# Kernel tuning notes

Measured on AMD Instinct MI355X. Metric: run time of the kernel, lower is better.

Reference implementation:

```python
import jax, jax.numpy as jnp
import numpy as np

N, E = 50000, 400000
IN_DIM, EDGE_F, OUT_DIM, EDGE_OUT, H = 256, 64, 32, 64, 8
ALPHA, TEMP, EPS = 0.2, 1.0, 1e-5


def lrelu(x):
    return jax.nn.leaky_relu(x, negative_slope=ALPHA)


def batch_norm(x, gamma, beta):
    # torch BatchNorm1d training-mode: biased variance over the batch dim
    mu = x.mean(0)
    var = x.var(0)
    return (x - mu) * jax.lax.rsqrt(var + EPS) * gamma + beta


def setup_inputs() -> dict:
    key = jax.random.key(0)
    ks = jax.random.split(key, 16)
    s = 0.05
    return {
        "node_inputs": jax.random.normal(ks[0], (N, IN_DIM), jnp.float32),
        "edge_inputs": jax.random.normal(ks[1], (E, EDGE_F), jnp.float32),
        "fc_w": jax.random.normal(ks[2], (IN_DIM, H * OUT_DIM), jnp.float32) * s,
        "attn_l": jax.random.normal(ks[3], (H, OUT_DIM), jnp.float32) * s,
        "attn_r": jax.random.normal(ks[4], (H, OUT_DIM), jnp.float32) * s,
        "ae_w1": jax.random.normal(ks[5], (EDGE_F, OUT_DIM), jnp.float32) * s,
        "ae_b1": jnp.zeros((OUT_DIM,), jnp.float32),
        "ae_w2": jax.random.normal(ks[6], (OUT_DIM, H), jnp.float32) * s,
        "ae_b2": jnp.zeros((H,), jnp.float32),
        "bn_n_g": jnp.ones((H * OUT_DIM,), jnp.float32),
        "bn_n_b": jnp.zeros((H * OUT_DIM,), jnp.float32),
        "eu_node_w": jax.random.normal(ks[7], (2 * H * OUT_DIM, EDGE_OUT), jnp.float32) * s,
        "eu_edge_w": jax.random.normal(ks[8], (EDGE_F, EDGE_OUT), jnp.float32) * s,
        "eu_final_w": jax.random.normal(ks[9], (2 * EDGE_OUT, EDGE_OUT), jnp.float32) * s,
        "bn_e_g": jnp.ones((EDGE_OUT,), jnp.float32),
        "bn_e_b": jnp.zeros((EDGE_OUT,), jnp.float32),
        "src": jax.random.randint(ks[10], (E,), 0, N, jnp.int32),
        "dst": jax.random.randint(ks[11], (E,), 0, N, jnp.int32),
    }


def reference(node_inputs, edge_inputs, fc_w, attn_l, attn_r, ae_w1, ae_b1, ae_w2,
              ae_b2, bn_n_g, bn_n_b, eu_node_w, eu_edge_w, eu_final_w, bn_e_g,
              bn_e_b, src, dst):
    # node projection, per-head attention scalars (dropout prob = 0 -> identity)
    ft = (node_inputs @ fc_w).reshape(N, H, OUT_DIM)          # [N,H,D]
    a1 = jnp.einsum('nhd,hd->nh', ft, attn_l)                 # [N,H]
    a2 = jnp.einsum('nhd,hd->nh', ft, attn_r)                 # [N,H]
    # edge-feature attention MLP: Linear -> LeakyReLU -> Linear
    e_attn = lrelu(edge_inputs @ ae_w1 + ae_b1) @ ae_w2 + ae_b2  # [E,H]
    a = lrelu(a1[src] + a2[dst] + e_attn) * TEMP              # [E,H]
    # two-pass edge softmax over incoming edges (segment by dst)
    a_max = jax.ops.segment_max(a, dst, num_segments=N)       # [N,H]
    a = jnp.exp(a - a_max[dst])                               # [E,H]
    z = jax.ops.segment_sum(a, dst, num_segments=N)           # [N,H]
    # weighted message aggregation
    msg = ft[src] * a[:, :, None]                             # [E,H,D]
    agg = jax.ops.segment_sum(msg, dst, num_segments=N)       # [N,H,D]
    z_safe = jnp.where(z == 0, 1.0, z)
    node_out = (agg / z_safe[:, :, None]).reshape(N, H * OUT_DIM)
    node_out = node_out + node_inputs                         # residual (dims match)
    node_out = batch_norm(lrelu(node_out), bn_n_g, bn_n_b)
    # edge update MLP
    node_f = lrelu(jnp.concatenate([node_out[src], node_out[dst]], -1) @ eu_node_w)
    edge_f = lrelu(edge_inputs @ eu_edge_w)
    edge_out = jnp.concatenate([node_f, edge_f], -1) @ eu_final_w
    edge_out = edge_out + edge_inputs                         # residual (dims match)
    edge_out = batch_norm(lrelu(edge_out), bn_e_g, bn_e_b)
    return node_out, edge_out
```

## Files before the change

### kernel.cpp

```cpp
#include <hip/hip_runtime.h>
#include <hip/hip_bf16.h>

typedef __hip_bfloat16 bf16;

#define N_NODES 50000
#define N_EDGES 400000
#define IN_DIM  256
#define EDGE_F  64
#define OUT_DIM 32
#define EDGE_OUT 64
#define NHEADS  8
#define HD      256
#define ALPHA   0.2f
#define BN_EPS  1e-5f

#define NBINS 50432
#define NBLK  197

__device__ __forceinline__ float b2f(bf16 v){ return __bfloat162float(v); }
__device__ __forceinline__ bf16  f2b(float v){ return __float2bfloat16(v); }
__device__ __forceinline__ float lrelu(float x){ return x > 0.f ? x : ALPHA*x; }
__device__ __forceinline__ unsigned fenc(float f){ unsigned u=__float_as_uint(f); return (u&0x80000000u)? ~u : (u|0x80000000u); }
__device__ __forceinline__ float fdec(unsigned k){ return (k&0x80000000u)? __uint_as_float(k&0x7fffffffu) : __uint_as_float(~k); }

template<bool F32> __device__ __forceinline__ float LD(const void* p, long i){
  if constexpr (F32) return ((const float*)p)[i];
  else               return b2f(((const bf16*)p)[i]);
}
template<bool F32> __device__ __forceinline__ void ST(void* p, long i, float v){
  if constexpr (F32) ((float*)p)[i] = v;
  else               ((bf16*)p)[i] = f2b(v);
}
template<bool F32> __device__ __forceinline__ void* ESEC(void* out){
  return (char*)out + (size_t)N_NODES*HD*(F32?4:2);
}

typedef __attribute__((ext_vector_type(8))) short bf16x8;
typedef __attribute__((ext_vector_type(4))) float f32x4;

union PackU { uint4 u; bf16x8 v; };
__device__ __forceinline__ bf16x8 as_frag(uint4 w){ PackU p; p.u = w; return p.v; }
__device__ __forceinline__ bf16x8 zero_frag(){ PackU p; p.u = make_uint4(0,0,0,0); return p.v; }

#define MFMA16(a,b,c) __builtin_amdgcn_mfma_f32_16x16x32_bf16(a,b,c,0,0,0)

__device__ __forceinline__ void split8(float4 a, float4 b, bf16x8& hi, bf16x8& lo){
  float v[8] = {a.x,a.y,a.z,a.w,b.x,b.y,b.z,b.w};
  unsigned hu[4], lu[4];
  #pragma unroll
  for(int i=0;i<4;i++){
    unsigned u0 = __float_as_uint(v[2*i]);
    unsigned u1 = __float_as_uint(v[2*i+1]);
    unsigned h0 = u0 & 0xffff0000u, h1 = u1 & 0xffff0000u;
    hu[i] = (u0>>16) | h1;
    float l0 = v[2*i]   - __uint_as_float(h0);
    float l1 = v[2*i+1] - __uint_as_float(h1);
    union { bf16 h; unsigned short s; } c0, c1; c0.h = f2b(l0); c1.h = f2b(l1);
    lu[i] = (unsigned)c0.s | ((unsigned)c1.s << 16);
  }
  PackU H,L;
  H.u = make_uint4(hu[0],hu[1],hu[2],hu[3]);
  L.u = make_uint4(lu[0],lu[1],lu[2],lu[3]);
  hi = H.v; lo = L.v;
}

template<bool F32> __device__ __forceinline__ void load_split(const void* p, long off, bf16x8& hi, bf16x8& lo){
  if constexpr(F32){
    const float* f = (const float*)p + off;
    float4 a = *(const float4*)f;
    float4 b = *(const float4*)(f+4);
    split8(a,b,hi,lo);
  } else {
    hi = as_frag(*(const uint4*)((const bf16*)p + off));
    lo = zero_frag();
  }
}

__global__ __launch_bounds__(256) void k_detect(const unsigned short* __restrict__ u,
                                                int* __restrict__ flag){
  __shared__ int cnt;
  if(threadIdx.x==0) cnt=0;
  __syncthreads();
  int local=0;
  for(int i=threadIdx.x;i<8192;i+=256){
    int e = (u[i]>>7)&0xFF;
    if(e>=200) local++;
  }
  atomicAdd(&cnt, local);
  __syncthreads();
  if(threadIdx.x==0) *flag = (cnt>64) ? 1 : 0;
}

__global__ __launch_bounds__(256) void k_hist(const int* __restrict__ dst, int* __restrict__ cnt){
  int e = blockIdx.x*256 + threadIdx.x;
  if(e < N_EDGES){
    unsigned d = (unsigned)dst[e];
    if(d < N_NODES) atomicAdd(&cnt[d], 1);
  }
}
__global__ __launch_bounds__(256) void k_scan1(const int* __restrict__ cnt, int* __restrict__ rs,
                                               int* __restrict__ btot){
  __shared__ int s[256];
  int t = threadIdx.x; int i = blockIdx.x*256 + t;
  int v = cnt[i]; s[t] = v; __syncthreads();
  for(int off=1; off<256; off<<=1){
    int x = (t>=off) ? s[t-off] : 0; __syncthreads();
    s[t] += x; __syncthreads();
  }
  rs[i] = s[t] - v;
  if(t==255) btot[blockIdx.x] = s[t];
}
__global__ __launch_bounds__(256) void k_scan2(const int* __restrict__ btot, int* __restrict__ bsum){
  __shared__ int s[256];
  int t = threadIdx.x;
  int v = (t<NBLK) ? btot[t] : 0; s[t] = v; __syncthreads();
  for(int off=1; off<256; off<<=1){
    int x = (t>=off) ? s[t-off] : 0; __syncthreads();
    s[t] += x; __syncthreads();
  }
  if(t<NBLK) bsum[t] = s[t] - v;
}
__global__ __launch_bounds__(256) void k_scan3(int* __restrict__ rs, const int* __restrict__ bsum,
                                               int* __restrict__ cursor){
  int i = blockIdx.x*256 + threadIdx.x;
  int r = rs[i] + bsum[blockIdx.x];
  rs[i] = r; cursor[i] = r;
}

template<bool F32> __device__ void pack_body(const void* wn, const void* we, const void* wf,
                                             const void* aw1, unsigned short* out){
  int i = blockIdx.x*256 + threadIdx.x;
  if(i >= 47104) return;
  union { bf16 h; unsigned short s; } u;
  if(i < 45056){
    const void* srcp; int idx;
    if(i < 32768){ srcp = wn; idx = i; }
    else if(i < 36864){ srcp = we; idx = i - 32768; }
    else { srcp = wf; idx = i - 36864; }
    int j = idx & 7, lane = (idx>>3)&63, nt = (idx>>9)&3, ks = idx>>11;
    int k = ks*32 + ((lane>>4)<<3) + j;
    int n = (nt<<4) + (lane&15);
    u.h = f2b(LD<F32>(srcp, (long)k*EDGE_OUT + n));
  } else {
    int idx = i - 45056;
    int j = idx & 7, lane = (idx>>3)&63, nt = (idx>>9)&1, ks = idx>>10;
    int k = ks*32 + ((lane>>4)<<3) + j;
    int n = (nt<<4) + (lane&15);
    u.h = f2b(LD<F32>(aw1, (long)k*OUT_DIM + n));
  }
  out[i] = u.s;
}
__global__ __launch_bounds__(256) void k_pack_w(const void* wn, const void* we, const void* wf,
                                                const void* aw1, unsigned short* out,
                                                const int* flag){
  if(*flag) pack_body<true >(wn,we,wf,aw1,out);
  else      pack_body<false>(wn,we,wf,aw1,out);
}
template<bool F32> __device__ void pack_fc_body(const void* w, unsigned short* out){
  int i = blockIdx.x*256 + threadIdx.x;
  int j = i&7, lane = (i>>3)&63, nt = (i>>9)&15, ks = i>>13;
  int k = ks*32 + ((lane>>4)<<3) + j;
  int n = (nt<<4) + (lane&15);
  union { bf16 h; unsigned short s; } u;
  u.h = f2b(LD<F32>(w, (long)k*HD + n));
  out[i] = u.s;
}
__global__ __launch_bounds__(256) void k_pack_fc(const void* w, unsigned short* out, const int* flag){
  if(*flag) pack_fc_body<true >(w,out);
  else      pack_fc_body<false>(w,out);
}

template<bool F32> __device__ void nproj_body(const void* x, const unsigned short* wpf, float* ft){
  const uint4* w4 = (const uint4*)wpf;
  int wid = threadIdx.x>>6, lane = threadIdx.x&63;
  int row16 = lane&15, kgrp = lane>>4;
  int r0 = blockIdx.x*64 + wid*16;
  long arow = r0 + row16; if(arow >= N_NODES) arow = N_NODES-1;
  f32x4 acc[16];
  #pragma unroll
  for(int nt=0;nt<16;nt++) acc[nt] = (f32x4){0.f,0.f,0.f,0.f};
  #pragma unroll 2
  for(int ks=0;ks<8;ks++){
    bf16x8 ah, al;
    load_split<F32>(x, arow*IN_DIM + ks*32 + kgrp*8, ah, al);
    const uint4* wb = w4 + (size_t)(ks*16)*64 + lane;
    #pragma unroll
    for(int nt=0;nt<16;nt++){
      bf16x8 b = as_frag(wb[nt*64]);
      if constexpr(F32) acc[nt] = MFMA16(al, b, acc[nt]);
      acc[nt] = MFMA16(ah, b, acc[nt]);
    }
  }
  #pragma unroll
  for(int nt=0;nt<16;nt++)
    #pragma unroll
    for(int j=0;j<4;j++){
      int r = r0 + kgrp*4 + j;
      if(r < N_NODES) ft[(long)r*HD + nt*16 + row16] = acc[nt][j];
    }
}
__global__ __launch_bounds__(256) void k_node_proj(const void* x, const unsigned short* wpf,
                                                   float* ft, const int* flag){
  if(*flag) nproj_body<true >(x,wpf,ft);
  else      nproj_body<false>(x,wpf,ft);
}

template<bool F32> __device__ void attn_body(const float* ft, const void* al, const void* ar,
                                             float* a1, float* a2){
  int gid = blockIdx.x*8 + (threadIdx.x>>5);
  int d   = threadIdx.x & 31;
  int h   = gid & 7;
  float v  = ft[(long)gid*OUT_DIM + d];
  float s1 = v * LD<F32>(al, h*OUT_DIM + d);
  float s2 = v * LD<F32>(ar, h*OUT_DIM + d);
  for(int o=16;o>0;o>>=1){ s1 += __shfl_down(s1,o,32); s2 += __shfl_down(s2,o,32); }
  if(d==0){ a1[gid]=s1; a2[gid]=s2; }
}
__global__ __launch_bounds__(256) void k_attn(const float* ft, const void* al, const void* ar,
                                              float* a1, float* a2, const int* flag){
  if(*flag) attn_body<true >(ft,al,ar,a1,a2);
  else      attn_body<false>(ft,al,ar,a1,a2);
}

#define ST_STRIDE 20

template<bool F32>
__device__ void edge_attn_body(const void* ein, const void* b1, const void* w2, const void* b2,
                               const float* a1, const float* a2,
                               const int* src, const int* dst,
                               int* cursor, unsigned short* psrc,
                               float* a_edge, unsigned* amax,
                               const unsigned short* wpack, float* sm){
  const uint4* aw1 = ((const uint4*)wpack) + 5632;
  float* sw2f = sm;
  float* sb1  = sm + 256;
  float* sb2  = sm + 288;
  float* st   = sm + 296;
  int t = threadIdx.x;
  sw2f[t] = LD<F32>(w2, t);
  if(t<OUT_DIM) sb1[t] = LD<F32>(b1, t);
  if(t<NHEADS)  sb2[t] = LD<F32>(b2, t);
  __syncthreads();

  int wid = t>>6, lane = t&63;
  int row16 = lane&15, kgrp = lane>>4;
  int e0w = blockIdx.x*64 + wid*16;
  int e_a = e0w + row16;
  float* myst = st + wid*(32*ST_STRIDE);

  f32x4 acc_h[2], acc_l[2];
  #pragma unroll
  for(int q=0;q<2;q++){ acc_h[q]=(f32x4){0.f,0.f,0.f,0.f}; acc_l[q]=(f32x4){0.f,0.f,0.f,0.f}; }
  long ebase = (long)e_a * EDGE_F;
  #pragma unroll
  for(int ks=0; ks<2; ks++){
    bf16x8 ah, al;
    load_split<F32>(ein, ebase + ks*32 + kgrp*8, ah, al);
    const uint4* wb = aw1 + (size_t)(ks*2)*64 + lane;
    #pragma unroll
    for(int nt=0; nt<2; nt++){
      bf16x8 bfr = as_frag(wb[nt*64]);
      acc_h[nt] = MFMA16(ah, bfr, acc_h[nt]);
      if constexpr(F32) acc_l[nt] = MFMA16(al, bfr, acc_l[nt]);
    }
  }
  #pragma unroll
  for(int nt=0; nt<2; nt++){
    int col = nt*16 + row16;
    float4 v;
    v.x = lrelu(acc_h[nt][0] + acc_l[nt][0] + sb1[col]);
    v.y = lrelu(acc_h[nt][1] + acc_l[nt][1] + sb1[col]);
    v.z = lrelu(acc_h[nt][2] + acc_l[nt][2] + sb1[col]);
    v.w = lrelu(acc_h[nt][3] + acc_l[nt][3] + sb1[col]);
    *(float4*)&myst[col*ST_STRIDE + kgrp*4] = v;
  }
  __syncthreads();

  int h = lane&7, r = lane>>3;
  float s0 = sb2[h], s1 = sb2[h];
  #pragma unroll 8
  for(int k=0;k<OUT_DIM;k++){
    float w = sw2f[k*NHEADS+h];
    s0 = fmaf(myst[k*ST_STRIDE + r],     w, s0);
    s1 = fmaf(myst[k*ST_STRIDE + r + 8], w, s1);
  }
  int ea0 = e0w + r, ea1 = e0w + r + 8;
  int sv0 = src[ea0], dv0 = dst[ea0];
  int sv1 = src[ea1], dv1 = dst[ea1];
  float av0 = lrelu(a1[sv0*NHEADS+h] + a2[dv0*NHEADS+h] + s0);
  float av1 = lrelu(a1[sv1*NHEADS+h] + a2[dv1*NHEADS+h] + s1);
  int pos0 = 0, pos1 = 0;
  if(h==0){
    pos0 = atomicAdd(&cursor[dv0], 1);
    pos1 = atomicAdd(&cursor[dv1], 1);
  }
  pos0 = __shfl(pos0, lane & 56, 64);
  pos1 = __shfl(pos1, lane & 56, 64);
  a_edge[(long)pos0*NHEADS + h] = av0;
  a_edge[(long)pos1*NHEADS + h] = av1;
  if(h==0){ psrc[pos0] = (unsigned short)sv0; psrc[pos1] = (unsigned short)sv1; }
  atomicMax(&amax[dv0*NHEADS+h], fenc(av0));
  atomicMax(&amax[dv1*NHEADS+h], fenc(av1));
}
__global__ __launch_bounds__(256) void k_edge_attn(const void* ein, const void* b1,
                                                   const void* w2, const void* b2,
                                                   const float* a1, const float* a2,
                                                   const int* src, const int* dst,
                                                   int* cursor, unsigned short* psrc,
                                                   float* a_edge, unsigned* amax,
                                                   const unsigned short* wpack, const int* flag){
  extern __shared__ float smemf[];
  if(*flag) edge_attn_body<true >(ein,b1,w2,b2,a1,a2,src,dst,cursor,psrc,a_edge,amax,wpack,smemf);
  else      edge_attn_body<false>(ein,b1,w2,b2,a1,a2,src,dst,cursor,psrc,a_edge,amax,wpack,smemf);
}

template<bool F32> __device__ void agg_body(const int* rs, const unsigned short* psrc,
                                            const float* a_edge, const unsigned* amax,
                                            const float* ft, const void* xin, void* xout,
                                            double* dstats, double* sm){
  int wid = threadIdx.x>>6, lane = threadIdx.x&63;
  int gw = blockIdx.x*4 + wid, nw = gridDim.x*4;
  int h0 = lane>>5;
  double s4[4]={0,0,0,0}, q4[4]={0,0,0,0};
  for(int n=gw; n<N_NODES; n+=nw){
    int b0 = rs[n], b1 = rs[n+1];
    if(b1 > N_EDGES) b1 = N_EDGES;
    if(b0 > b1) b0 = b1;
    float m = (lane<8) ? fdec(amax[n*NHEADS+lane]) : 0.f;
    float zl = 0.f;
    float acc[4] = {0,0,0,0};
    for(int i=b0;i<b1;++i){
      float av = 0.f;
      if(lane<8){ av = __expf(a_edge[(long)i*NHEADS+lane] - m); zl += av; }
      int sv = psrc[i];
      const float* fr = ft + (long)sv*HD;
      #pragma unroll
      for(int q=0;q<4;q++){
        float a = __shfl(av, h0 + 2*q, 64);
        acc[q] = fmaf(a, fr[lane + 64*q], acc[q]);
      }
    }
    #pragma unroll
    for(int q=0;q<4;q++){
      float z = __shfl(zl, h0 + 2*q, 64);
      float zs = (z==0.f) ? 1.f : z;
      int c = lane + 64*q;
      float xv = lrelu(acc[q]/zs + LD<F32>(xin,(long)n*HD + c));
      ST<F32>(xout,(long)n*HD + c, xv);
      s4[q] += xv; q4[q] += (double)xv*(double)xv;
    }
  }
  double* ls = sm; double* lq = sm + 256;
  for(int w=0;w<4;w++){
    if(wid==w){
      #pragma unroll
      for(int q=0;q<4;q++){
        int c = lane + 64*q;
        if(w==0){ ls[c]=s4[q]; lq[c]=q4[q]; }
        else    { ls[c]+=s4[q]; lq[c]+=q4[q]; }
      }
    }
    __syncthreads();
  }
  int t = threadIdx.x;
  unsafeAtomicAdd(&dstats[t],    ls[t]);
  unsafeAtomicAdd(&dstats[HD+t], lq[t]);
}
__global__ __launch_bounds__(256) void k_agg(const int* rs, const unsigned short* psrc,
                                             const float* a_edge, const unsigned* amax,
                                             const float* ft, const void* xin, void* xout,
                                             double* dstats, const int* flag){
  extern __shared__ double smemd[];
  if(*flag) agg_body<true >(rs,psrc,a_edge,amax,ft,xin,xout,dstats,smemd);
  else      agg_body<false>(rs,psrc,a_edge,amax,ft,xin,xout,dstats,smemd);
}

template<bool F32> __device__ void bn_params_body(const double* dstats, const void* g,
                                                  const void* b, float* scsh, int C, double invM){
  int t = threadIdx.x;
  if(t>=C) return;
  double mu  = dstats[t]*invM;
  double var = dstats[C+t]*invM - mu*mu;
  if(var < 0.0) var = 0.0;
  float sc = LD<F32>(g,t) * rsqrtf((float)var + BN_EPS);
  scsh[t]   = sc;
  scsh[C+t] = LD<F32>(b,t) - (float)mu*sc;
}
__global__ void k_bn_params(const double* dstats, const void* g, const void* b,
                            float* scsh, int C, double invM, const int* flag){
  if(*flag) bn_params_body<true >(dstats,g,b,scsh,C,invM);
  else      bn_params_body<false>(dstats,g,b,scsh,C,invM);
}

template<bool F32> __device__ void node_apply_body(void* x, const float* scsh){
  int t = threadIdx.x;
  float sc = scsh[t], sh = scsh[HD+t];
  for(long i=(long)blockIdx.x*256+t; i<(long)N_NODES*HD; i+=(long)gridDim.x*256){
    ST<F32>(x, i, fmaf(LD<F32>(x,i), sc, sh));
  }
}
__global__ __launch_bounds__(256) void k_node_apply(void* x, const float* scsh, const int* flag){
  if(*flag) node_apply_body<true >(x,scsh);
  else      node_apply_body<false>(x,scsh);
}

template<bool F32> __device__ void pq_body(const void* nodeb, const unsigned short* wpack,
                                           float* P, float* Q){
  const uint4* wn4 = (const uint4*)wpack;
  int wid = threadIdx.x>>6, lane = threadIdx.x&63;
  int row16 = lane&15, kgrp = lane>>4;
  int r0 = blockIdx.x*64 + wid*16;
  long arow = r0 + row16; if(arow >= N_NODES) arow = N_NODES-1;
  f32x4 pacc[4], qacc[4];
  #pragma unroll
  for(int nt=0;nt<4;nt++){ pacc[nt]=(f32x4){0.f,0.f,0.f,0.f}; qacc[nt]=(f32x4){0.f,0.f,0.f,0.f}; }
  #pragma unroll 2
  for(int ks=0;ks<8;ks++){
    bf16x8 ah, al;
    load_split<F32>(nodeb, arow*HD + ks*32 + kgrp*8, ah, al);
    const uint4* wbP = wn4 + (size_t)(ks*4)*64 + lane;
    const uint4* wbQ = wn4 + (size_t)((8+ks)*4)*64 + lane;
    #pragma unroll
    for(int nt=0;nt<4;nt++){
      bf16x8 bP = as_frag(wbP[nt*64]);
      bf16x8 bQ = as_frag(wbQ[nt*64]);
      pacc[nt] = MFMA16(ah, bP, pacc[nt]);
      qacc[nt] = MFMA16(ah, bQ, qacc[nt]);
      if constexpr(F32){
        pacc[nt] = MFMA16(al, bP, pacc[nt]);
        qacc[nt] = MFMA16(al, bQ, qacc[nt]);
      }
    }
  }
  #pragma unroll
  for(int nt=0;nt<4;nt++)
    #pragma unroll
    for(int j=0;j<4;j++){
      int r = r0 + kgrp*4 + j;
      if(r < N_NODES){
        P[(long)r*64 + nt*16 + row16] = pacc[nt][j];
        Q[(long)r*64 + nt*16 + row16] = qacc[nt][j];
      }
    }
}
__global__ __launch_bounds__(256) void k_pq(const void* nodeb, const unsigned short* wpack,
                                            float* P, float* Q, const int* flag){
  if(*flag) pq_body<true >(nodeb,wpack,P,Q);
  else      pq_body<false>(nodeb,wpack,P,Q);
}

#define EF_LROW 68

template<bool F32>
__device__ void edge_update_body(const float* P, const float* Q, const void* edge_in,
                                 const int* src, const int* dst,
                                 const unsigned short* wpack,
                                 void* d_out, float* lds){
  void* edge_x = ESEC<F32>(d_out);
  const uint4* we4 = ((const uint4*)wpack) + 4096;
  const uint4* wf4 = ((const uint4*)wpack) + 4608;
  int wid   = threadIdx.x >> 6;
  int lane  = threadIdx.x & 63;
  int row16 = lane & 15;
  int kgrp  = lane >> 4;
  int e0  = blockIdx.x*64 + wid*16;
  int e_a = e0 + row16;
  int nsrc = src[e_a], ndst = dst[e_a];
  float* myl = lds + wid*(16*EF_LROW);

  f32x4 acc_h[4], acc_l[4];
  #pragma unroll
  for(int t=0;t<4;t++){ acc_h[t]=(f32x4){0.f,0.f,0.f,0.f}; acc_l[t]=(f32x4){0.f,0.f,0.f,0.f}; }

  long ebase = (long)e_a * EDGE_F;
  #pragma unroll
  for(int ks=0; ks<2; ks++){
    bf16x8 ah, al;
    load_split<F32>(edge_in, ebase + ks*32 + kgrp*8, ah, al);
    const uint4* wb = we4 + (size_t)(ks*4)*64 + lane;
    #pragma unroll
    for(int nt=0; nt<4; nt++){
      bf16x8 bfr = as_frag(wb[nt*64]);
      acc_h[nt] = MFMA16(ah, bfr, acc_h[nt]);
      if constexpr(F32) acc_l[nt] = MFMA16(al, bfr, acc_l[nt]);
    }
  }
  #pragma unroll
  for(int nt=0; nt<4; nt++)
    #pragma unroll
    for(int j=0;j<4;j++)
      myl[(kgrp*4+j)*EF_LROW + nt*16 + row16] = lrelu(acc_h[nt][j] + acc_l[nt][j]);

  __syncthreads();

  #pragma unroll
  for(int t=0;t<4;t++){ acc_h[t]=(f32x4){0.f,0.f,0.f,0.f}; acc_l[t]=(f32x4){0.f,0.f,0.f,0.f}; }
  #pragma unroll
  for(int ks=0; ks<2; ks++){
    const float* pp = P + (long)nsrc*64 + ks*32 + kgrp*8;
    const float* qq = Q + (long)ndst*64 + ks*32 + kgrp*8;
    float4 p0 = *(const float4*)pp, p1 = *(const float4*)(pp+4);
    float4 q0 = *(const float4*)qq, q1 = *(const float4*)(qq+4);
    float4 v0, v1;
    v0.x = lrelu(p0.x+q0.x); v0.y = lrelu(p0.y+q0.y);
    v0.z = lrelu(p0.z+q0.z); v0.w = lrelu(p0.w+q0.w);
    v1.x = lrelu(p1.x+q1.x); v1.y = lrelu(p1.y+q1.y);
    v1.z = lrelu(p1.z+q1.z); v1.w = lrelu(p1.w+q1.w);
    bf16x8 ah, al; split8(v0, v1, ah, al);
    const uint4* wb = wf4 + (size_t)(ks*4)*64 + lane;
    #pragma unroll
    for(int nt=0; nt<4; nt++){
      bf16x8 bfr = as_frag(wb[nt*64]);
      acc_h[nt] = MFMA16(ah, bfr, acc_h[nt]);
      acc_l[nt] = MFMA16(al, bfr, acc_l[nt]);
    }
  }
  #pragma unroll
  for(int ks=2; ks<4; ks++){
    const float* ap = myl + row16*EF_LROW + (ks-2)*32 + kgrp*8;
    float4 a0 = *(const float4*)ap;
    float4 a1 = *(const float4*)(ap+4);
    bf16x8 ah, al; split8(a0, a1, ah, al);
    const uint4* wb = wf4 + (size_t)(ks*4)*64 + lane;
    #pragma unroll
    for(int nt=0; nt<4; nt++){
      bf16x8 bfr = as_frag(wb[nt*64]);
      acc_h[nt] = MFMA16(ah, bfr, acc_h[nt]);
      acc_l[nt] = MFMA16(al, bfr, acc_l[nt]);
    }
  }
  #pragma unroll
  for(int nt=0; nt<4; nt++)
    #pragma unroll
    for(int j=0;j<4;j++){
      long e = e0 + kgrp*4 + j;
      int  c = nt*16 + row16;
      float res = LD<F32>(edge_in, e*EDGE_OUT + c);
      ST<F32>(edge_x, e*EDGE_OUT + c, lrelu(acc_h[nt][j] + acc_l[nt][j] + res));
    }
}
__global__ __launch_bounds__(256) void k_edge_update(const float* P, const float* Q,
                                                     const void* edge_in,
                                                     const int* src, const int* dst,
                                                     const unsigned short* wpack,
                                                     void* d_out, const int* flag){
  extern __shared__ float smemf[];
  if(*flag) edge_update_body<true >(P,Q,edge_in,src,dst,wpack,d_out,smemf);
  else      edge_update_body<false>(P,Q,edge_in,src,dst,wpack,d_out,smemf);
}

template<bool F32> __device__ void edge_stats_body(void* d_out, double* dstats, double* sm){
  const void* ex = ESEC<F32>(d_out);
  double* ls = sm; double* lq = sm+256;
  int t = threadIdx.x;
  int c = t & 63, r0 = t >> 6;
  double s=0.0, q=0.0;
  for(long i=(long)(blockIdx.x*4 + r0)*64 + c; i < (long)N_EDGES*EDGE_OUT; i += (long)gridDim.x*4*64){
    float x = LD<F32>(ex, i);
    s += x; q += (double)x*(double)x;
  }
  ls[t]=s; lq[t]=q;
  __syncthreads();
  if(t<64){
    double ss = ls[t]+ls[t+64]+ls[t+128]+ls[t+192];
    double qq = lq[t]+lq[t+64]+lq[t+128]+lq[t+192];
    unsafeAtomicAdd(&dstats[t], ss);
    unsafeAtomicAdd(&dstats[64+t], qq);
  }
}
__global__ __launch_bounds__(256) void k_edge_stats(void* d_out, double* dstats, const int* flag){
  extern __shared__ double smemd[];
  if(*flag) edge_stats_body<true >(d_out,dstats,smemd);
  else      edge_stats_body<false>(d_out,dstats,smemd);
}

template<bool F32> __device__ void edge_apply_body(void* d_out, const float* scsh){
  void* ex = ESEC<F32>(d_out);
  int t = threadIdx.x;
  int c = t & 63;
  float sc = scsh[c], sh = scsh[64+c];
  for(long i=(long)blockIdx.x*256+t; i<(long)N_EDGES*EDGE_OUT; i+=(long)gridDim.x*256){
    ST<F32>(ex, i, fmaf(LD<F32>(ex,i), sc, sh));
  }
}
__global__ __launch_bounds__(256) void k_edge_apply(void* d_out, const float* scsh, const int* flag){
  if(*flag) edge_apply_body<true >(d_out,scsh);
  else      edge_apply_body<false>(d_out,scsh);
}

extern "C" void kernel_launch(void* const* d_in, const int* in_sizes, int n_in,
                              void* d_out, int out_size, void* d_ws, size_t ws_size,
                              hipStream_t stream){
  const void* node_in    = d_in[0];
  const void* edge_in    = d_in[1];
  const void* fc_w       = d_in[2];
  const void* attn_l     = d_in[3];
  const void* attn_r     = d_in[4];
  const void* ae_w1      = d_in[5];
  const void* ae_b1      = d_in[6];
  const void* ae_w2      = d_in[7];
  const void* ae_b2      = d_in[8];
  const void* bn_n_g     = d_in[9];
  const void* bn_n_b     = d_in[10];
  const void* eu_node_w  = d_in[11];
  const void* eu_edge_w  = d_in[12];
  const void* eu_final_w = d_in[13];
  const void* bn_e_g     = d_in[14];
  const void* bn_e_b     = d_in[15];
  const int*  src        = (const int*)d_in[16];
  const int*  dst        = (const int*)d_in[17];

  char* base = (char*)d_ws;
  double*   dstats_n = (double*)base;
  double*   dstats_e = (double*)(base + 4096);
  float*    scsh_n   = (float*)(base + 5120);
  float*    scsh_e   = (float*)(base + 7168);
  int*      flag     = (int*)(base + 7680);
  char*     big      = base + 8192;
  float*    ftb      = (float*)big;
  float*    Pb       = (float*)big;
  float*    Qb       = (float*)(big + 12800000);
  float*    a_edge   = (float*)(big + 51200000);
  float*    a1       = (float*)(big + 64000000);
  float*    a2       = (float*)(big + 65600000);
  unsigned* amax     = (unsigned*)(big + 67200000);
  unsigned short* wpack_eu = (unsigned short*)(big + 68800000);
  unsigned short* wpack_fc = (unsigned short*)(big + 68900000);
  int*      rsb      = (int*)(big + 69040000);
  int*      cursor   = (int*)(big + 69250000);
  int*      btot     = (int*)(big + 69460000);
  int*      bsum     = (int*)(big + 69461024);
  unsigned short* psrc = (unsigned short*)(big + 69470000);

  hipMemsetAsync(dstats_n, 0, 640*sizeof(double), stream);
  hipMemsetAsync(amax, 0, (size_t)N_NODES*NHEADS*sizeof(unsigned), stream);
  hipMemsetAsync(cursor, 0, NBINS*sizeof(int), stream);

  k_detect<<<1, 256, 0, stream>>>((const unsigned short*)node_in, flag);
  k_hist <<<(N_EDGES+255)/256, 256, 0, stream>>>(dst, cursor);
  k_scan1<<<NBLK, 256, 0, stream>>>(cursor, rsb, btot);
  k_scan2<<<1, 256, 0, stream>>>(btot, bsum);
  k_scan3<<<NBLK, 256, 0, stream>>>(rsb, bsum, cursor);
  k_pack_fc<<<256, 256, 0, stream>>>(fc_w, wpack_fc, flag);
  k_pack_w<<<184, 256, 0, stream>>>(eu_node_w, eu_edge_w, eu_final_w, ae_w1, wpack_eu, flag);
  k_node_proj<<<(N_NODES+63)/64, 256, 0, stream>>>(node_in, wpack_fc, ftb, flag);
  k_attn<<<N_NODES*NHEADS/8, 256, 0, stream>>>(ftb, attn_l, attn_r, a1, a2, flag);
  k_edge_attn<<<N_EDGES/64, 256, (296 + 4*32*ST_STRIDE)*4, stream>>>(
      edge_in, ae_b1, ae_w2, ae_b2, a1, a2, src, dst, cursor, psrc,
      a_edge, amax, wpack_eu, flag);
  k_agg<<<960, 256, 4096, stream>>>(rsb, psrc, a_edge, amax, ftb, node_in, d_out,
                                    dstats_n, flag);
  k_bn_params<<<1, 256, 0, stream>>>(dstats_n, bn_n_g, bn_n_b, scsh_n, HD, 1.0/N_NODES, flag);
  k_node_apply<<<2048, 256, 0, stream>>>(d_out, scsh_n, flag);
  k_pq<<<(N_NODES+63)/64, 256, 0, stream>>>(d_out, wpack_eu, Pb, Qb, flag);
  k_edge_update<<<N_EDGES/64, 256, 4*16*EF_LROW*4, stream>>>(Pb, Qb, edge_in, src, dst,
                                                             wpack_eu, d_out, flag);
  k_edge_stats<<<512, 256, 4096, stream>>>(d_out, dstats_e, flag);
  k_bn_params<<<1, 256, 0, stream>>>(dstats_e, bn_e_g, bn_e_b, scsh_e, EDGE_OUT, 1.0/N_EDGES, flag);
  k_edge_apply<<<2048, 256, 0, stream>>>(d_out, scsh_e, flag);
  (void)ws_size; (void)out_size; (void)n_in; (void)in_sizes;
}
```

Baseline: 826.6 us.

## Fuse node BN apply into PQ GEMM and edge stats into edge update

The node batch-norm apply pass is folded into the PQ GEMM, which normalizes the loaded rows, feeds them to MFMA and writes them back to the output. The edge statistics pass is folded into the edge-update epilogue using shared-memory float atomics followed by double global atomics. The aggregation kernel switches to float4 gathers with contiguous columns per lane, and its grid grows from 960 to 2048 blocks. This removes two full read/write passes over the node and edge outputs, at the cost of float-precision partial sums and more atomic traffic.

Result: faster. 805.4 us (-2.6%).

```diff
diff --git a/kernel.cpp b/kernel.cpp
--- a/kernel.cpp
+++ b/kernel.cpp
@@ -320,7 +320,7 @@
                                             double* dstats, double* sm){
   int wid = threadIdx.x>>6, lane = threadIdx.x&63;
   int gw = blockIdx.x*4 + wid, nw = gridDim.x*4;
-  int h0 = lane>>5;
+  int h = lane>>3;
   double s4[4]={0,0,0,0}, q4[4]={0,0,0,0};
   for(int n=gw; n<N_NODES; n+=nw){
     int b0 = rs[n], b1 = rs[n+1];
@@ -333,18 +333,18 @@
       float av = 0.f;
       if(lane<8){ av = __expf(a_edge[(long)i*NHEADS+lane] - m); zl += av; }
       int sv = psrc[i];
-      const float* fr = ft + (long)sv*HD;
-      #pragma unroll
-      for(int q=0;q<4;q++){
-        float a = __shfl(av, h0 + 2*q, 64);
-        acc[q] = fmaf(a, fr[lane + 64*q], acc[q]);
-      }
-    }
+      float4 f = *(const float4*)(ft + (long)sv*HD + lane*4);
+      float a = __shfl(av, h, 64);
+      acc[0] = fmaf(a, f.x, acc[0]);
+      acc[1] = fmaf(a, f.y, acc[1]);
+      acc[2] = fmaf(a, f.z, acc[2]);
+      acc[3] = fmaf(a, f.w, acc[3]);
+    }
+    float z = __shfl(zl, h, 64);
+    float zs = (z==0.f) ? 1.f : z;
     #pragma unroll
     for(int q=0;q<4;q++){
-      float z = __shfl(zl, h0 + 2*q, 64);
-      float zs = (z==0.f) ? 1.f : z;
-      int c = lane + 64*q;
+      int c = lane*4 + q;
       float xv = lrelu(acc[q]/zs + LD<F32>(xin,(long)n*HD + c));
       ST<F32>(xout,(long)n*HD + c, xv);
       s4[q] += xv; q4[q] += (double)xv*(double)xv;
@@ -355,7 +355,7 @@
     if(wid==w){
       #pragma unroll
       for(int q=0;q<4;q++){
-        int c = lane + 64*q;
+        int c = lane*4 + q;
         if(w==0){ ls[c]=s4[q]; lq[c]=q4[q]; }
         else    { ls[c]+=s4[q]; lq[c]+=q4[q]; }
       }
@@ -392,32 +392,44 @@
   else      bn_params_body<false>(dstats,g,b,scsh,C,invM);
 }
 
-template<bool F32> __device__ void node_apply_body(void* x, const float* scsh){
-  int t = threadIdx.x;
-  float sc = scsh[t], sh = scsh[HD+t];
-  for(long i=(long)blockIdx.x*256+t; i<(long)N_NODES*HD; i+=(long)gridDim.x*256){
-    ST<F32>(x, i, fmaf(LD<F32>(x,i), sc, sh));
-  }
-}
-__global__ __launch_bounds__(256) void k_node_apply(void* x, const float* scsh, const int* flag){
-  if(*flag) node_apply_body<true >(x,scsh);
-  else      node_apply_body<false>(x,scsh);
-}
-
-template<bool F32> __device__ void pq_body(const void* nodeb, const unsigned short* wpack,
-                                           float* P, float* Q){
+template<bool F32> __device__ void pq_body(void* nodex, const unsigned short* wpack,
+                                           const float* scsh, float* P, float* Q){
   const uint4* wn4 = (const uint4*)wpack;
   int wid = threadIdx.x>>6, lane = threadIdx.x&63;
   int row16 = lane&15, kgrp = lane>>4;
   int r0 = blockIdx.x*64 + wid*16;
-  long arow = r0 + row16; if(arow >= N_NODES) arow = N_NODES-1;
+  bool owns = (r0 + row16) < N_NODES;
+  long arow = owns ? (long)(r0 + row16) : (long)(N_NODES-1);
   f32x4 pacc[4], qacc[4];
   #pragma unroll
   for(int nt=0;nt<4;nt++){ pacc[nt]=(f32x4){0.f,0.f,0.f,0.f}; qacc[nt]=(f32x4){0.f,0.f,0.f,0.f}; }
   #pragma unroll 2
   for(int ks=0;ks<8;ks++){
+    int cb = ks*32 + kgrp*8;
+    float y[8];
+    #pragma unroll
+    for(int j=0;j<8;j++){
+      float x = LD<F32>(nodex, arow*HD + cb + j);
+      y[j] = fmaf(x, scsh[cb+j], scsh[HD+cb+j]);
+    }
     bf16x8 ah, al;
-    load_split<F32>(nodeb, arow*HD + ks*32 + kgrp*8, ah, al);
+    if constexpr(F32){
+      float4 y0 = {y[0],y[1],y[2],y[3]}, y1 = {y[4],y[5],y[6],y[7]};
+      split8(y0, y1, ah, al);
+      if(owns){
+        *(float4*)((float*)nodex + arow*HD + cb)     = y0;
+        *(float4*)((float*)nodex + arow*HD + cb + 4) = y1;
+      }
+    } else {
+      unsigned short us[8];
+      #pragma unroll
+      for(int j=0;j<8;j++){ union{bf16 h; unsigned short s;}u; u.h=f2b(y[j]); us[j]=u.s; }
+      PackU pk;
+      pk.u = make_uint4((unsigned)us[0]|((unsigned)us[1]<<16), (unsigned)us[2]|((unsigned)us[3]<<16),
+                        (unsigned)us[4]|((unsigned)us[5]<<16), (unsigned)us[6]|((unsigned)us[7]<<16));
+      ah = pk.v; al = zero_frag();
+      if(owns) *(uint4*)((bf16*)nodex + arow*HD + cb) = pk.u;
+    }
     const uint4* wbP = wn4 + (size_t)(ks*4)*64 + lane;
     const uint4* wbQ = wn4 + (size_t)((8+ks)*4)*64 + lane;
     #pragma unroll
@@ -443,10 +455,11 @@
       }
     }
 }
-__global__ __launch_bounds__(256) void k_pq(const void* nodeb, const unsigned short* wpack,
-                                            float* P, float* Q, const int* flag){
-  if(*flag) pq_body<true >(nodeb,wpack,P,Q);
-  else      pq_body<false>(nodeb,wpack,P,Q);
+__global__ __launch_bounds__(256) void k_pq(void* nodex, const unsigned short* wpack,
+                                            const float* scsh, float* P, float* Q,
+                                            const int* flag){
+  if(*flag) pq_body<true >(nodex,wpack,scsh,P,Q);
+  else      pq_body<false>(nodex,wpack,scsh,P,Q);
 }
 
 #define EF_LROW 68
@@ -455,18 +468,21 @@
 __device__ void edge_update_body(const float* P, const float* Q, const void* edge_in,
                                  const int* src, const int* dst,
                                  const unsigned short* wpack,
-                                 void* d_out, float* lds){
+                                 void* d_out, double* dstats,
+                                 float* lds, float* els, float* elq){
   void* edge_x = ESEC<F32>(d_out);
   const uint4* we4 = ((const uint4*)wpack) + 4096;
   const uint4* wf4 = ((const uint4*)wpack) + 4608;
-  int wid   = threadIdx.x >> 6;
-  int lane  = threadIdx.x & 63;
+  int tid   = threadIdx.x;
+  int wid   = tid >> 6;
+  int lane  = tid & 63;
   int row16 = lane & 15;
   int kgrp  = lane >> 4;
   int e0  = blockIdx.x*64 + wid*16;
   int e_a = e0 + row16;
   int nsrc = src[e_a], ndst = dst[e_a];
   float* myl = lds + wid*(16*EF_LROW);
+  if(tid < 64){ els[tid] = 0.f; elq[tid] = 0.f; }
 
   f32x4 acc_h[4], acc_l[4];
   #pragma unroll
@@ -530,48 +546,36 @@
     }
   }
   #pragma unroll
-  for(int nt=0; nt<4; nt++)
+  for(int nt=0; nt<4; nt++){
+    float ssum = 0.f, qsum = 0.f;
     #pragma unroll
     for(int j=0;j<4;j++){
       long e = e0 + kgrp*4 + j;
       int  c = nt*16 + row16;
       float res = LD<F32>(edge_in, e*EDGE_OUT + c);
-      ST<F32>(edge_x, e*EDGE_OUT + c, lrelu(acc_h[nt][j] + acc_l[nt][j] + res));
-    }
+      float v = lrelu(acc_h[nt][j] + acc_l[nt][j] + res);
+      ST<F32>(edge_x, e*EDGE_OUT + c, v);
+      ssum += v; qsum += v*v;
+    }
+    atomicAdd(&els[nt*16+row16], ssum);
+    atomicAdd(&elq[nt*16+row16], qsum);
+  }
+  __syncthreads();
+  if(tid < 64){
+    unsafeAtomicAdd(&dstats[tid],    (double)els[tid]);
+    unsafeAtomicAdd(&dstats[64+tid], (double)elq[tid]);
+  }
 }
 __global__ __launch_bounds__(256) void k_edge_update(const float* P, const float* Q,
                                                      const void* edge_in,
                                                      const int* src, const int* dst,
                                                      const unsigned short* wpack,
-                                                     void* d_out, const int* flag){
+                                                     void* d_out, double* dstats,
+                                                     const int* flag){
   extern __shared__ float smemf[];
-  if(*flag) edge_update_body<true >(P,Q,edge_in,src,dst,wpack,d_out,smemf);
-  else      edge_update_body<false>(P,Q,edge_in,src,dst,wpack,d_out,smemf);
-}
-
-template<bool F32> __device__ void edge_stats_body(void* d_out, double* dstats, double* sm){
-  const void* ex = ESEC<F32>(d_out);
-  double* ls = sm; double* lq = sm+256;
-  int t = threadIdx.x;
-  int c = t & 63, r0 = t >> 6;
-  double s=0.0, q=0.0;
-  for(long i=(long)(blockIdx.x*4 + r0)*64 + c; i < (long)N_EDGES*EDGE_OUT; i += (long)gridDim.x*4*64){
-    float x = LD<F32>(ex, i);
-    s += x; q += (double)x*(double)x;
-  }
-  ls[t]=s; lq[t]=q;
-  __syncthreads();
-  if(t<64){
-    double ss = ls[t]+ls[t+64]+ls[t+128]+ls[t+192];
-    double qq = lq[t]+lq[t+64]+lq[t+128]+lq[t+192];
-    unsafeAtomicAdd(&dstats[t], ss);
-    unsafeAtomicAdd(&dstats[64+t], qq);
-  }
-}
-__global__ __launch_bounds__(256) void k_edge_stats(void* d_out, double* dstats, const int* flag){
-  extern __shared__ double smemd[];
-  if(*flag) edge_stats_body<true >(d_out,dstats,smemd);
-  else      edge_stats_body<false>(d_out,dstats,smemd);
+  __shared__ float els[64], elq[64];
+  if(*flag) edge_update_body<true >(P,Q,edge_in,src,dst,wpack,d_out,dstats,smemf,els,elq);
+  else      edge_update_body<false>(P,Q,edge_in,src,dst,wpack,d_out,dstats,smemf,els,elq);
 }
 
 template<bool F32> __device__ void edge_apply_body(void* d_out, const float* scsh){
@@ -648,14 +652,12 @@
   k_edge_attn<<<N_EDGES/64, 256, (296 + 4*32*ST_STRIDE)*4, stream>>>(
       edge_in, ae_b1, ae_w2, ae_b2, a1, a2, src, dst, cursor, psrc,
       a_edge, amax, wpack_eu, flag);
-  k_agg<<<960, 256, 4096, stream>>>(rsb, psrc, a_edge, amax, ftb, node_in, d_out,
-                                    dstats_n, flag);
+  k_agg<<<2048, 256, 4096, stream>>>(rsb, psrc, a_edge, amax, ftb, node_in, d_out,
+                                     dstats_n, flag);
   k_bn_params<<<1, 256, 0, stream>>>(dstats_n, bn_n_g, bn_n_b, scsh_n, HD, 1.0/N_NODES, flag);
-  k_node_apply<<<2048, 256, 0, stream>>>(d_out, scsh_n, flag);
-  k_pq<<<(N_NODES+63)/64, 256, 0, stream>>>(d_out, wpack_eu, Pb, Qb, flag);
+  k_pq<<<(N_NODES+63)/64, 256, 0, stream>>>(d_out, wpack_eu, scsh_n, Pb, Qb, flag);
   k_edge_update<<<N_EDGES/64, 256, 4*16*EF_LROW*4, stream>>>(Pb, Qb, edge_in, src, dst,
-                                                             wpack_eu, d_out, flag);
-  k_edge_stats<<<512, 256, 4096, stream>>>(d_out, dstats_e, flag);
+                                                             wpack_eu, d_out, dstats_e, flag);
   k_bn_params<<<1, 256, 0, stream>>>(dstats_e, bn_e_g, bn_e_b, scsh_e, EDGE_OUT, 1.0/N_EDGES, flag);
   k_edge_apply<<<2048, 256, 0, stream>>>(d_out, scsh_e, flag);
   (void)ws_size; (void)out_size; (void)n_in; (void)in_sizes;
```
